# Performance work log

Hardware: AMD Instinct MI355X
Metric: run time of the kernel (lower is better)

## Reference

```python
import jax, jax.numpy as jnp
import numpy as np

H = W = 56
WS = 7            # window size
SHIFT = 3
HEADS = 6
DIM = 192
N = WS * WS       # tokens per window (49)
NW = (H // WS) * (W // WS)  # windows per image (64)
EPS = 1e-5


def _rel_pos_index():
    coords = np.stack(np.meshgrid(np.arange(WS), np.arange(WS), indexing='ij'))
    cf = coords.reshape(2, -1)
    rel = (cf[:, :, None] - cf[:, None, :]).transpose(1, 2, 0)
    rel[:, :, 0] += WS - 1
    rel[:, :, 1] += WS - 1
    rel[:, :, 0] *= 2 * WS - 1
    return rel.sum(-1).astype(np.int32)  # [N, N]


def _attn_mask():
    img = np.zeros([1, H, W, 1], dtype=np.float32)
    slices = (slice(0, -WS), slice(-WS, -SHIFT), slice(-SHIFT, None))
    cnt = 0
    for hs in slices:
        for ws_ in slices:
            img[:, hs, ws_, :] = cnt
            cnt += 1
    m = img.reshape(1, H // WS, WS, W // WS, WS, 1).transpose(0, 1, 3, 2, 4, 5)
    m = m.reshape(-1, N)                      # [nW, N]
    diff = m[:, None, :] - m[:, :, None]
    return np.where(diff != 0, -100.0, 0.0).astype(np.float32)  # [nW, N, N]

_RPI = _rel_pos_index()
_MASK = _attn_mask()


def _ln(x, g, b):
    mu = jnp.mean(x, axis=-1, keepdims=True)
    var = jnp.mean(jnp.square(x - mu), axis=-1, keepdims=True)
    return (x - mu) * jax.lax.rsqrt(var + EPS) * g + b


def setup_inputs() -> dict:
    key = jax.random.key(0)
    ks = jax.random.split(key, 12)
    C, Hd = DIM, DIM * 4
    s = lambda n: 1.0 / np.sqrt(n)
    return {
        'x': jax.random.normal(ks[0], (32, H * W, C), jnp.float32),
        'norm1_g': jnp.ones((C,), jnp.float32),
        'norm1_b': jnp.zeros((C,), jnp.float32),
        'qkv_w': jax.random.normal(ks[1], (C, 3 * C), jnp.float32) * s(C),
        'qkv_b': jnp.zeros((3 * C,), jnp.float32),
        'bias_table': jax.random.normal(ks[2], ((2 * WS - 1) ** 2, HEADS), jnp.float32) * 0.02,
        'proj_w': jax.random.normal(ks[3], (C, C), jnp.float32) * s(C),
        'proj_b': jnp.zeros((C,), jnp.float32),
        'norm2_g': jnp.ones((C,), jnp.float32),
        'norm2_b': jnp.zeros((C,), jnp.float32),
        'fc1_w': jax.random.normal(ks[4], (C, Hd), jnp.float32) * s(C),
        'fc1_b': jnp.zeros((Hd,), jnp.float32),
        'fc2_w': jax.random.normal(ks[5], (Hd, C), jnp.float32) * s(Hd),
        'fc2_b': jnp.zeros((C,), jnp.float32),
    }


def reference(x, norm1_g, norm1_b, qkv_w, qkv_b, bias_table, proj_w, proj_b,
              norm2_g, norm2_b, fc1_w, fc1_b, fc2_w, fc2_b):
    B, L, C = x.shape
    hd = C // HEADS
    scale = hd ** -0.5

    shortcut = x
    h = _ln(x, norm1_g, norm1_b).reshape(B, H, W, C)
    h = jnp.roll(h, (-SHIFT, -SHIFT), axis=(1, 2))

    # window partition -> [B*nW, N, C]
    h = h.reshape(B, H // WS, WS, W // WS, WS, C).transpose(0, 1, 3, 2, 4, 5)
    xw = h.reshape(B * NW, N, C)

    qkv = (xw @ qkv_w + qkv_b).reshape(B * NW, N, 3, HEADS, hd)
    q, k, v = jnp.moveaxis(qkv, 2, 0)                 # each [B*nW, N, H, d]
    q = jnp.swapaxes(q, 1, 2) * scale                 # [B*nW, H, N, d]
    k = jnp.swapaxes(k, 1, 2)
    v = jnp.swapaxes(v, 1, 2)

    attn = jnp.einsum('whnd,whmd->whnm', q, k)        # [B*nW, H, N, N]
    bias = bias_table[jnp.asarray(_RPI).reshape(-1)].reshape(N, N, HEADS)
    attn = attn + jnp.transpose(bias, (2, 0, 1))[None]
    mask = jnp.asarray(_MASK)                         # [nW, N, N]
    attn = attn.reshape(B, NW, HEADS, N, N) + mask[None, :, None]
    attn = jax.nn.softmax(attn.reshape(B * NW, HEADS, N, N), axis=-1)

    out = jnp.einsum('whnm,whmd->whnd', attn, v)      # [B*nW, H, N, d]
    out = jnp.swapaxes(out, 1, 2).reshape(B * NW, N, C)
    out = out @ proj_w + proj_b

    # window reverse -> [B, H, W, C]
    out = out.reshape(B, H // WS, W // WS, WS, WS, C).transpose(0, 1, 3, 2, 4, 5)
    out = out.reshape(B, H, W, C)
    out = jnp.roll(out, (SHIFT, SHIFT), axis=(1, 2)).reshape(B, L, C)

    x = shortcut + out
    hmlp = _ln(x, norm2_g, norm2_b)
    hmlp = jax.nn.gelu(hmlp @ fc1_w + fc1_b, approximate=False) @ fc2_w + fc2_b
    return x + hmlp
```

## Files before the change

kernel.cpp:

```cpp
#include <hip/hip_runtime.h>
#include <hip/hip_bf16.h>
#include <math.h>

static constexpr int CB     = 32;
static constexpr int CH     = 56;
static constexpr int CW     = 56;
static constexpr int CC     = 192;
static constexpr int CSHIFT = 3;
static constexpr int CN     = 49;
static constexpr int CNW    = 64;
static constexpr int CL     = CH * CW;
static constexpr int CM     = CB * CNW * CN;
static constexpr int CHID   = 768;

typedef __attribute__((ext_vector_type(8))) __bf16 bf16x8;
typedef __attribute__((ext_vector_type(4))) float  f32x4;

__device__ __forceinline__ float bfu2f(unsigned short u) {
  union { unsigned i; float f; } c; c.i = (unsigned)u << 16; return c.f;
}
__device__ __forceinline__ unsigned short f2bu(float f) {
  __hip_bfloat16 b = __float2bfloat16(f);
  return *(unsigned short*)&b;
}
__device__ __forceinline__ float gelu_fast(float v) {
  float s  = v * v;
  float u2 = v * fmaf(s, 0.0713548163f, 1.5957691216f);
  float e  = __expf(u2);
  float t  = 1.0f - __fdividef(2.0f, e + 1.0f);
  float h  = 0.5f * v;
  return fmaf(h, t, h);
}

#define GLOAD16(g, l) __builtin_amdgcn_global_load_lds( \
    (__attribute__((address_space(1))) void*)(g),       \
    (__attribute__((address_space(3))) void*)(l), 16, 0, 0)

__global__ __launch_bounds__(256)
void prep_kernel(const float* __restrict__ qkv_w, const float* __restrict__ proj_w,
                 const float* __restrict__ fc1_w, const float* __restrict__ fc2_w,
                 const float* __restrict__ btab,
                 __hip_bfloat16* __restrict__ wq, __hip_bfloat16* __restrict__ wp,
                 __hip_bfloat16* __restrict__ w1, __hip_bfloat16* __restrict__ w2,
                 float* __restrict__ bias2)
{
  int idx = blockIdx.x * 256 + threadIdx.x;
  if (idx < 110592) {
    int k = idx / 576, n = idx - k * 576;
    wq[n * 192 + k] = __float2bfloat16(qkv_w[idx]);
    return;
  }
  idx -= 110592;
  if (idx < 36864) {
    int k = idx / 192, n = idx - k * 192;
    wp[n * 192 + k] = __float2bfloat16(proj_w[idx]);
    return;
  }
  idx -= 36864;
  if (idx < 147456) {
    int k = idx / 768, n = idx - k * 768;
    w1[n * 192 + k] = __float2bfloat16(fc1_w[idx]);
    return;
  }
  idx -= 147456;
  if (idx < 147456) {
    int k = idx / 192, n = idx - k * 192;
    w2[n * 768 + k] = __float2bfloat16(fc2_w[idx]);
    return;
  }
  idx -= 147456;
  if (idx < 98304) {
    int j = idx & 63, i = (idx >> 6) & 63;
    int rest = idx >> 12;
    int h = rest % 6, wt = rest / 6;
    float val;
    if (i >= 49 || j >= 49) {
      val = -INFINITY;
    } else {
      int ti = i / 7, ci = i - ti * 7;
      int tj = j / 7, cj = j - tj * 7;
      val = btab[((ti - tj + 6) * 13 + (ci - cj + 6)) * 6 + h];
      int hri = (wt & 2) ? ((ti < 4) ? 1 : 2) : 0;
      int hci = (wt & 1) ? ((ci < 4) ? 1 : 2) : 0;
      int hrj = (wt & 2) ? ((tj < 4) ? 1 : 2) : 0;
      int hcj = (wt & 1) ? ((cj < 4) ? 1 : 2) : 0;
      if (hri * 3 + hci != hrj * 3 + hcj) val -= 100.0f;
    }
    bias2[idx] = val;
  }
}

template<bool ROLL>
__global__ __launch_bounds__(256)
void ln_kernel(const float* __restrict__ xin, const float* __restrict__ gamma,
               const float* __restrict__ beta, __hip_bfloat16* __restrict__ out)
{
  const int wid = threadIdx.x >> 6, lane = threadIdx.x & 63;
  const int m = blockIdx.x * 4 + wid;
  size_t src;
  if (ROLL) {
    int b   = m / (CNW * CN);
    int rem = m - b * (CNW * CN);
    int nw  = rem / CN, t = rem - nw * CN;
    int wr = nw >> 3, wc = nw & 7;
    int ti = t / 7, tj = t - ti * 7;
    int sr = wr * 7 + ti + CSHIFT; if (sr >= CH) sr -= CH;
    int sc = wc * 7 + tj + CSHIFT; if (sc >= CW) sc -= CW;
    src = ((size_t)b * CL + (size_t)sr * CW + sc) * CC;
  } else {
    src = (size_t)m * CC;
  }
  float v0 = xin[src + lane], v1 = xin[src + lane + 64], v2 = xin[src + lane + 128];
  float s  = v0 + v1 + v2;
  float sq = v0 * v0 + v1 * v1 + v2 * v2;
  #pragma unroll
  for (int off = 32; off; off >>= 1) { s += __shfl_xor(s, off); sq += __shfl_xor(sq, off); }
  const float mu  = s * (1.0f / CC);
  const float inv = rsqrtf(sq * (1.0f / CC) - mu * mu + 1e-5f);
  const size_t dst = (size_t)m * CC;
  out[dst + lane      ] = __float2bfloat16((v0 - mu) * inv * gamma[lane      ] + beta[lane      ]);
  out[dst + lane + 64 ] = __float2bfloat16((v1 - mu) * inv * gamma[lane + 64 ] + beta[lane + 64 ]);
  out[dst + lane + 128] = __float2bfloat16((v2 - mu) * inv * gamma[lane + 128] + beta[lane + 128]);
}

template<int MODE>
__global__ __launch_bounds__(256)
void gemm_mfma(const __hip_bfloat16* __restrict__ Ain, const __hip_bfloat16* __restrict__ Wt,
               const float* __restrict__ bias, void* __restrict__ Outv,
               const float* __restrict__ resid, int K, int Ncols)
{
  __shared__ short As[256 * 64];
  __shared__ short Bs[64 * 64];

  const int tid  = threadIdx.x;
  const int lane = tid & 63, wid = tid >> 6;

  const int nbx = gridDim.x;
  const int nwg = nbx * gridDim.y;
  const int wg  = blockIdx.y * nbx + blockIdx.x;
  const int swz = (wg & 7) * (nwg >> 3) + (wg >> 3);
  const int row0 = (swz / nbx) * 256, col0 = (swz % nbx) * 64;

  const int lr = lane & 15, lg = lane >> 4;

  const short* A  = (const short*)Ain;
  const short* W  = (const short*)Wt;

  f32x4 acc[4][4] = {};

  for (int kk = 0; kk < K; kk += 64) {
    #pragma unroll
    for (int it = 0; it < 8; ++it) {
      int c = it * 256 + tid;
      int row = c >> 3, slot = c & 7;
      int kg = (slot ^ (row & 7)) * 8;
      GLOAD16(A + (size_t)(row0 + row) * K + kk + kg, As + c * 8);
    }
    #pragma unroll
    for (int it = 0; it < 2; ++it) {
      int c = it * 256 + tid;
      int row = c >> 3, slot = c & 7;
      int kg = (slot ^ (row & 7)) * 8;
      GLOAD16(W + (size_t)(col0 + row) * K + kk + kg, Bs + c * 8);
    }
    __syncthreads();

    #pragma unroll
    for (int kh = 0; kh < 2; ++kh) {
      const int sb = kh * 4 + lg;
      bf16x8 bfr[4];
      #pragma unroll
      for (int nt = 0; nt < 4; ++nt) {
        int br = nt * 16 + lr;
        bfr[nt] = *(const bf16x8*)(Bs + br * 64 + (sb ^ (br & 7)) * 8);
      }
      #pragma unroll
      for (int m = 0; m < 4; ++m) {
        int ar = wid * 64 + m * 16 + lr;
        bf16x8 afr = *(const bf16x8*)(As + ar * 64 + (sb ^ (ar & 7)) * 8);
        #pragma unroll
        for (int nt = 0; nt < 4; ++nt)
          acc[m][nt] = __builtin_amdgcn_mfma_f32_16x16x32_bf16(afr, bfr[nt], acc[m][nt], 0, 0, 0);
      }
    }
    __syncthreads();
  }

  float bv[4];
  #pragma unroll
  for (int nt = 0; nt < 4; ++nt) bv[nt] = bias[col0 + nt * 16 + lr];

  #pragma unroll
  for (int m = 0; m < 4; ++m) {
    #pragma unroll
    for (int r = 0; r < 4; ++r) {
      const int mrow = row0 + wid * 64 + m * 16 + lg * 4 + r;
      if (MODE == 0) {
        __hip_bfloat16* O = (__hip_bfloat16*)Outv;
        const size_t rr = (size_t)mrow * Ncols + col0 + lr;
        #pragma unroll
        for (int nt = 0; nt < 4; ++nt)
          O[rr + nt * 16] = __float2bfloat16(acc[m][nt][r] + bv[nt]);
      } else if (MODE == 1) {
        int b = mrow / (CNW * CN);
        int rem = mrow - b * (CNW * CN);
        int nw = rem / CN, t = rem - nw * CN;
        int wr = nw >> 3, wc = nw & 7;
        int ti = t / 7, tj = t - ti * 7;
        int dr = wr * 7 + ti + CSHIFT; if (dr >= CH) dr -= CH;
        int dc = wc * 7 + tj + CSHIFT; if (dc >= CW) dc -= CW;
        const size_t dst = ((size_t)b * CL + (size_t)dr * CW + dc) * CC + col0 + lr;
        float* O = (float*)Outv;
        #pragma unroll
        for (int nt = 0; nt < 4; ++nt)
          O[dst + nt * 16] = resid[dst + nt * 16] + acc[m][nt][r] + bv[nt];
      } else if (MODE == 2) {
        __hip_bfloat16* O = (__hip_bfloat16*)Outv;
        const size_t rr = (size_t)mrow * Ncols + col0 + lr;
        #pragma unroll
        for (int nt = 0; nt < 4; ++nt)
          O[rr + nt * 16] = __float2bfloat16(gelu_fast(acc[m][nt][r] + bv[nt]));
      } else {
        float* O = (float*)Outv;
        const size_t rr = (size_t)mrow * Ncols + col0 + lr;
        #pragma unroll
        for (int nt = 0; nt < 4; ++nt)
          O[rr + nt * 16] = resid[rr + nt * 16] + acc[m][nt][r] + bv[nt];
      }
    }
  }
}

__global__ __launch_bounds__(64)
void attn_mfma_kernel(const __hip_bfloat16* __restrict__ qkv,
                      const float* __restrict__ bias2,
                      __hip_bfloat16* __restrict__ attnout)
{
  __shared__ unsigned short VT[32 * 72];
  __shared__ unsigned short Pl[64 * 72];

  const int bid = blockIdx.x;
  const int w = bid / 6, h = bid - (bid / 6) * 6;
  const int lane = threadIdx.x;
  const int lr = lane & 15, lg = lane >> 4;
  const int nw = w & 63;
  const int wt = (((nw >> 3) == 7) ? 2 : 0) + (((nw & 7) == 7) ? 1 : 0);
  const unsigned short* Q = (const unsigned short*)qkv;
  const size_t rowbase = (size_t)w * 49 * 576;
  const float scale = 0.17677669529663687f;

  for (int e = lane; e < 196; e += 64) {
    int t = e % 49, c = e / 49;
    uint4 v = *(const uint4*)(Q + rowbase + (size_t)t * 576 + 384 + h * 32 + c * 8);
    unsigned va[4] = {v.x, v.y, v.z, v.w};
    #pragma unroll
    for (int q = 0; q < 4; ++q) {
      VT[(c * 8 + q * 2    ) * 72 + t] = (unsigned short)(va[q] & 0xffff);
      VT[(c * 8 + q * 2 + 1) * 72 + t] = (unsigned short)(va[q] >> 16);
    }
  }
  for (int e = lane; e < 32 * 15; e += 64) {
    int d = e / 15, t = 49 + e - (e / 15) * 15;
    VT[d * 72 + t] = 0;
  }

  bf16x8 qf[4], kf[4];
  #pragma unroll
  for (int it = 0; it < 4; ++it) {
    int tok = it * 16 + lr; if (tok > 48) tok = 48;
    qf[it] = *(const bf16x8*)(Q + rowbase + (size_t)tok * 576 + h * 32 + lg * 8);
  }
  #pragma unroll
  for (int jt = 0; jt < 4; ++jt) {
    int tok = jt * 16 + lr; if (tok > 48) tok = 48;
    kf[jt] = *(const bf16x8*)(Q + rowbase + (size_t)tok * 576 + 192 + h * 32 + lg * 8);
  }

  f32x4 acc[4][4] = {};
  #pragma unroll
  for (int jt = 0; jt < 4; ++jt)
    #pragma unroll
    for (int it = 0; it < 4; ++it)
      acc[jt][it] = __builtin_amdgcn_mfma_f32_16x16x32_bf16(kf[jt], qf[it], acc[jt][it], 0, 0, 0);

  __syncthreads();

  const float* brow = bias2 + ((size_t)(wt * 6 + h) * 64) * 64;
  #pragma unroll
  for (int it = 0; it < 4; ++it) {
    const int i = it * 16 + lr;
    float s[4][4];
    #pragma unroll
    for (int jt = 0; jt < 4; ++jt) {
      float4 bv = *(const float4*)(brow + (size_t)i * 64 + jt * 16 + lg * 4);
      s[jt][0] = fmaf(acc[jt][it][0], scale, bv.x);
      s[jt][1] = fmaf(acc[jt][it][1], scale, bv.y);
      s[jt][2] = fmaf(acc[jt][it][2], scale, bv.z);
      s[jt][3] = fmaf(acc[jt][it][3], scale, bv.w);
    }
    float mx = s[0][0];
    #pragma unroll
    for (int jt = 0; jt < 4; ++jt)
      #pragma unroll
      for (int r = 0; r < 4; ++r) mx = fmaxf(mx, s[jt][r]);
    mx = fmaxf(mx, __shfl_xor(mx, 16));
    mx = fmaxf(mx, __shfl_xor(mx, 32));
    float sum = 0.0f;
    #pragma unroll
    for (int jt = 0; jt < 4; ++jt)
      #pragma unroll
      for (int r = 0; r < 4; ++r) { s[jt][r] = __expf(s[jt][r] - mx); sum += s[jt][r]; }
    sum += __shfl_xor(sum, 16);
    sum += __shfl_xor(sum, 32);
    const float inv = 1.0f / sum;
    #pragma unroll
    for (int jt = 0; jt < 4; ++jt) {
      unsigned lo = (unsigned)f2bu(s[jt][0] * inv) | ((unsigned)f2bu(s[jt][1] * inv) << 16);
      unsigned hi = (unsigned)f2bu(s[jt][2] * inv) | ((unsigned)f2bu(s[jt][3] * inv) << 16);
      uint2 val; val.x = lo; val.y = hi;
      *(uint2*)&Pl[i * 72 + jt * 16 + lg * 4] = val;
    }
  }

  __syncthreads();

  f32x4 o[4][2] = {};
  #pragma unroll
  for (int ks = 0; ks < 2; ++ks) {
    bf16x8 pa[4], vb[2];
    #pragma unroll
    for (int it = 0; it < 4; ++it)
      pa[it] = *(const bf16x8*)&Pl[(it * 16 + lr) * 72 + ks * 32 + lg * 8];
    #pragma unroll
    for (int nt = 0; nt < 2; ++nt)
      vb[nt] = *(const bf16x8*)&VT[(nt * 16 + lr) * 72 + ks * 32 + lg * 8];
    #pragma unroll
    for (int it = 0; it < 4; ++it) {
      o[it][0] = __builtin_amdgcn_mfma_f32_16x16x32_bf16(pa[it], vb[0], o[it][0], 0, 0, 0);
      o[it][1] = __builtin_amdgcn_mfma_f32_16x16x32_bf16(pa[it], vb[1], o[it][1], 0, 0, 0);
    }
  }

  #pragma unroll
  for (int it = 0; it < 4; ++it) {
    #pragma unroll
    for (int r = 0; r < 4; ++r) {
      int i = it * 16 + lg * 4 + r;
      if (i < 49) {
        size_t dst = ((size_t)w * 49 + i) * 192 + h * 32;
        attnout[dst + lr]      = __float2bfloat16(o[it][0][r]);
        attnout[dst + 16 + lr] = __float2bfloat16(o[it][1][r]);
      }
    }
  }
}

extern "C" void kernel_launch(void* const* d_in, const int* in_sizes, int n_in,
                              void* d_out, int out_size, void* d_ws, size_t ws_size,
                              hipStream_t stream)
{
  const float* x        = (const float*)d_in[0];
  const float* n1g      = (const float*)d_in[1];
  const float* n1b      = (const float*)d_in[2];
  const float* qkv_w    = (const float*)d_in[3];
  const float* qkv_b    = (const float*)d_in[4];
  const float* btab     = (const float*)d_in[5];
  const float* proj_w   = (const float*)d_in[6];
  const float* proj_b   = (const float*)d_in[7];
  const float* n2g      = (const float*)d_in[8];
  const float* n2b      = (const float*)d_in[9];
  const float* fc1_w    = (const float*)d_in[10];
  const float* fc1_b    = (const float*)d_in[11];
  const float* fc2_w    = (const float*)d_in[12];
  const float* fc2_b    = (const float*)d_in[13];
  float* out = (float*)d_out;

  char* ws = (char*)d_ws;
  const size_t szA = (size_t)CM * CC * 2;
  const size_t szB = (size_t)CM * CHID * 2;
  __hip_bfloat16* bufA = (__hip_bfloat16*)ws;
  __hip_bfloat16* bufB = (__hip_bfloat16*)(ws + szA);
  __hip_bfloat16* wq   = (__hip_bfloat16*)(ws + szA + szB);
  __hip_bfloat16* wp   = wq + 576 * 192;
  __hip_bfloat16* w1   = wp + 192 * 192;
  __hip_bfloat16* w2   = w1 + 768 * 192;
  float* bias2         = (float*)(w2 + 192 * 768);

  prep_kernel<<<(110592 + 36864 + 147456 + 147456 + 98304 + 255) / 256, 256, 0, stream>>>(
      qkv_w, proj_w, fc1_w, fc2_w, btab, wq, wp, w1, w2, bias2);

  ln_kernel<true><<<CM / 4, 256, 0, stream>>>(x, n1g, n1b, bufA);
  gemm_mfma<0><<<dim3(576 / 64, CM / 256), 256, 0, stream>>>(bufA, wq, qkv_b, bufB, nullptr, CC, 576);
  attn_mfma_kernel<<<2048 * 6, 64, 0, stream>>>(bufB, bias2, bufA);
  gemm_mfma<1><<<dim3(192 / 64, CM / 256), 256, 0, stream>>>(bufA, wp, proj_b, out, x, CC, 192);
  ln_kernel<false><<<CM / 4, 256, 0, stream>>>(out, n2g, n2b, bufA);
  gemm_mfma<2><<<dim3(CHID / 64, CM / 256), 256, 0, stream>>>(bufA, w1, fc1_b, bufB, nullptr, CC, CHID);
  gemm_mfma<3><<<dim3(192 / 64, CM / 256), 256, 0, stream>>>(bufB, w2, fc2_b, out, out, CHID, 192);
}
```

Baseline: 369.3 us.

## Replace LDS-staged GEMM with register-direct per-wave 64x64 tiles

The shared-memory tiled GEMM, which used async global-to-LDS loads and block barriers, is replaced by a kernel where each wave independently computes a 64x64 output tile. A and B fragments are loaded straight from global memory into registers with double buffering, and K is now a template parameter so the k-loop fully unrolls. This removes LDS traffic and __syncthreads, but waves no longer share A rows across a block, so global and L2 traffic rises and loads are strided per lane.

New measurement: 511.0 us. +38.4%, slower.

```diff
diff --git a/kernel.cpp b/kernel.cpp
--- a/kernel.cpp
+++ b/kernel.cpp
@@ -31,10 +31,6 @@
   float h  = 0.5f * v;
   return fmaf(h, t, h);
 }
-
-#define GLOAD16(g, l) __builtin_amdgcn_global_load_lds( \
-    (__attribute__((address_space(1))) void*)(g),       \
-    (__attribute__((address_space(3))) void*)(l), 16, 0, 0)
 
 __global__ __launch_bounds__(256)
 void prep_kernel(const float* __restrict__ qkv_w, const float* __restrict__ proj_w,
@@ -123,67 +119,52 @@
   out[dst + lane + 128] = __float2bfloat16((v2 - mu) * inv * gamma[lane + 128] + beta[lane + 128]);
 }
 
-template<int MODE>
+template<int K, int MODE>
 __global__ __launch_bounds__(256)
-void gemm_mfma(const __hip_bfloat16* __restrict__ Ain, const __hip_bfloat16* __restrict__ Wt,
-               const float* __restrict__ bias, void* __restrict__ Outv,
-               const float* __restrict__ resid, int K, int Ncols)
-{
-  __shared__ short As[256 * 64];
-  __shared__ short Bs[64 * 64];
-
-  const int tid  = threadIdx.x;
-  const int lane = tid & 63, wid = tid >> 6;
-
-  const int nbx = gridDim.x;
-  const int nwg = nbx * gridDim.y;
-  const int wg  = blockIdx.y * nbx + blockIdx.x;
-  const int swz = (wg & 7) * (nwg >> 3) + (wg >> 3);
-  const int row0 = (swz / nbx) * 256, col0 = (swz % nbx) * 64;
-
+void gemm_reg(const __hip_bfloat16* __restrict__ Ain, const __hip_bfloat16* __restrict__ Wt,
+              const float* __restrict__ bias, void* __restrict__ Outv,
+              const float* __restrict__ resid, int Ncols)
+{
+  const int tid = threadIdx.x, lane = tid & 63, wid = tid >> 6;
   const int lr = lane & 15, lg = lane >> 4;
 
-  const short* A  = (const short*)Ain;
-  const short* W  = (const short*)Wt;
-
+  const int nb   = gridDim.x;
+  const int sbid = (blockIdx.x & 7) * (nb >> 3) + (blockIdx.x >> 3);
+  const int nbx  = Ncols >> 6;
+  const int t    = sbid * 4 + wid;
+  const int trow = t / nbx;
+  const int row0 = trow * 64, col0 = (t - trow * nbx) * 64;
+
+  const short* A = (const short*)Ain;
+  const short* W = (const short*)Wt;
+  const short* ap = A + (size_t)(row0 + lr) * K + lg * 8;
+  const short* bp = W + (size_t)(col0 + lr) * K + lg * 8;
+
+  constexpr int NK = K / 32;
   f32x4 acc[4][4] = {};
-
-  for (int kk = 0; kk < K; kk += 64) {
-    #pragma unroll
-    for (int it = 0; it < 8; ++it) {
-      int c = it * 256 + tid;
-      int row = c >> 3, slot = c & 7;
-      int kg = (slot ^ (row & 7)) * 8;
-      GLOAD16(A + (size_t)(row0 + row) * K + kk + kg, As + c * 8);
-    }
-    #pragma unroll
-    for (int it = 0; it < 2; ++it) {
-      int c = it * 256 + tid;
-      int row = c >> 3, slot = c & 7;
-      int kg = (slot ^ (row & 7)) * 8;
-      GLOAD16(W + (size_t)(col0 + row) * K + kk + kg, Bs + c * 8);
-    }
-    __syncthreads();
-
-    #pragma unroll
-    for (int kh = 0; kh < 2; ++kh) {
-      const int sb = kh * 4 + lg;
-      bf16x8 bfr[4];
-      #pragma unroll
-      for (int nt = 0; nt < 4; ++nt) {
-        int br = nt * 16 + lr;
-        bfr[nt] = *(const bf16x8*)(Bs + br * 64 + (sb ^ (br & 7)) * 8);
-      }
-      #pragma unroll
-      for (int m = 0; m < 4; ++m) {
-        int ar = wid * 64 + m * 16 + lr;
-        bf16x8 afr = *(const bf16x8*)(As + ar * 64 + (sb ^ (ar & 7)) * 8);
-        #pragma unroll
-        for (int nt = 0; nt < 4; ++nt)
-          acc[m][nt] = __builtin_amdgcn_mfma_f32_16x16x32_bf16(afr, bfr[nt], acc[m][nt], 0, 0, 0);
-      }
-    }
-    __syncthreads();
+  bf16x8 af[2][4], bf[2][4];
+
+  #pragma unroll
+  for (int m = 0; m < 4; ++m) af[0][m] = *(const bf16x8*)(ap + (size_t)m * 16 * K);
+  #pragma unroll
+  for (int n = 0; n < 4; ++n) bf[0][n] = *(const bf16x8*)(bp + (size_t)n * 16 * K);
+
+  #pragma unroll
+  for (int ks = 0; ks < NK; ++ks) {
+    const int cur = ks & 1, nxt = cur ^ 1;
+    if (ks + 1 < NK) {
+      #pragma unroll
+      for (int m = 0; m < 4; ++m)
+        af[nxt][m] = *(const bf16x8*)(ap + (size_t)m * 16 * K + (ks + 1) * 32);
+      #pragma unroll
+      for (int n = 0; n < 4; ++n)
+        bf[nxt][n] = *(const bf16x8*)(bp + (size_t)n * 16 * K + (ks + 1) * 32);
+    }
+    #pragma unroll
+    for (int m = 0; m < 4; ++m)
+      #pragma unroll
+      for (int n = 0; n < 4; ++n)
+        acc[m][n] = __builtin_amdgcn_mfma_f32_16x16x32_bf16(af[cur][m], bf[cur][n], acc[m][n], 0, 0, 0);
   }
 
   float bv[4];
@@ -194,7 +175,7 @@
   for (int m = 0; m < 4; ++m) {
     #pragma unroll
     for (int r = 0; r < 4; ++r) {
-      const int mrow = row0 + wid * 64 + m * 16 + lg * 4 + r;
+      const int mrow = row0 + m * 16 + lg * 4 + r;
       if (MODE == 0) {
         __hip_bfloat16* O = (__hip_bfloat16*)Outv;
         const size_t rr = (size_t)mrow * Ncols + col0 + lr;
@@ -204,9 +185,9 @@
       } else if (MODE == 1) {
         int b = mrow / (CNW * CN);
         int rem = mrow - b * (CNW * CN);
-        int nw = rem / CN, t = rem - nw * CN;
+        int nw = rem / CN, tt = rem - nw * CN;
         int wr = nw >> 3, wc = nw & 7;
-        int ti = t / 7, tj = t - ti * 7;
+        int ti = tt / 7, tj = tt - ti * 7;
         int dr = wr * 7 + ti + CSHIFT; if (dr >= CH) dr -= CH;
         int dc = wc * 7 + tj + CSHIFT; if (dc >= CW) dc -= CW;
         const size_t dst = ((size_t)b * CL + (size_t)dr * CW + dc) * CC + col0 + lr;
@@ -390,10 +371,10 @@
       qkv_w, proj_w, fc1_w, fc2_w, btab, wq, wp, w1, w2, bias2);
 
   ln_kernel<true><<<CM / 4, 256, 0, stream>>>(x, n1g, n1b, bufA);
-  gemm_mfma<0><<<dim3(576 / 64, CM / 256), 256, 0, stream>>>(bufA, wq, qkv_b, bufB, nullptr, CC, 576);
+  gemm_reg<192, 0><<<(CM / 64) * (576 / 64) / 4, 256, 0, stream>>>(bufA, wq, qkv_b, bufB, nullptr, 576);
   attn_mfma_kernel<<<2048 * 6, 64, 0, stream>>>(bufB, bias2, bufA);
-  gemm_mfma<1><<<dim3(192 / 64, CM / 256), 256, 0, stream>>>(bufA, wp, proj_b, out, x, CC, 192);
+  gemm_reg<192, 1><<<(CM / 64) * (192 / 64) / 4, 256, 0, stream>>>(bufA, wp, proj_b, out, x, 192);
   ln_kernel<false><<<CM / 4, 256, 0, stream>>>(out, n2g, n2b, bufA);
-  gemm_mfma<2><<<dim3(CHID / 64, CM / 256), 256, 0, stream>>>(bufA, w1, fc1_b, bufB, nullptr, CC, CHID);
-  gemm_mfma<3><<<dim3(192 / 64, CM / 256), 256, 0, stream>>>(bufB, w2, fc2_b, out, out, CHID, 192);
-}
+  gemm_reg<192, 2><<<(CM / 64) * (CHID / 64) / 4, 256, 0, stream>>>(bufA, w1, fc1_b, bufB, nullptr, CHID);
+  gemm_reg<768, 3><<<(CM / 64) * (192 / 64) / 4, 256, 0, stream>>>(bufB, w2, fc2_b, out, out, 192);
+}
```

## Retile GEMMs to 128-row blocks with 2x2 warp layout and compile-time shapes

Applied to the files above, without the earlier changes.

The GEMM kernel moves from 256x64 tiles, where each warp owns 64 rows by 64 columns, to 128xBN tiles (BN of 128 or 64) with a 2x2 warp grid. K and N become template parameters so the K loop can be fully unrolled. The QKV output is padded from 576 to 640 columns, with zeroed weights and bias, so its N divides by 128, and the attention kernel's row stride is changed to match. This aims to raise the number of workgroups and improve occupancy, at the cost of the extra padded QKV columns and a larger QKV buffer.

Result: faster. 349.3 us (-5.4%).

```diff
diff --git a/kernel.cpp b/kernel.cpp
--- a/kernel.cpp
+++ b/kernel.cpp
@@ -12,6 +12,7 @@
 static constexpr int CL     = CH * CW;
 static constexpr int CM     = CB * CNW * CN;
 static constexpr int CHID   = 768;
+static constexpr int QST    = 640;
 
 typedef __attribute__((ext_vector_type(8))) __bf16 bf16x8;
 typedef __attribute__((ext_vector_type(4))) float  f32x4;
@@ -39,18 +40,18 @@
 __global__ __launch_bounds__(256)
 void prep_kernel(const float* __restrict__ qkv_w, const float* __restrict__ proj_w,
                  const float* __restrict__ fc1_w, const float* __restrict__ fc2_w,
-                 const float* __restrict__ btab,
+                 const float* __restrict__ btab, const float* __restrict__ qkv_b,
                  __hip_bfloat16* __restrict__ wq, __hip_bfloat16* __restrict__ wp,
                  __hip_bfloat16* __restrict__ w1, __hip_bfloat16* __restrict__ w2,
-                 float* __restrict__ bias2)
+                 float* __restrict__ bias2, float* __restrict__ qkv_bp)
 {
   int idx = blockIdx.x * 256 + threadIdx.x;
-  if (idx < 110592) {
-    int k = idx / 576, n = idx - k * 576;
-    wq[n * 192 + k] = __float2bfloat16(qkv_w[idx]);
+  if (idx < QST * 192) {
+    int n = idx / 192, k = idx - n * 192;
+    wq[idx] = (n < 576) ? __float2bfloat16(qkv_w[k * 576 + n]) : __float2bfloat16(0.0f);
     return;
   }
-  idx -= 110592;
+  idx -= QST * 192;
   if (idx < 36864) {
     int k = idx / 192, n = idx - k * 192;
     wp[n * 192 + k] = __float2bfloat16(proj_w[idx]);
@@ -87,6 +88,11 @@
       if (hri * 3 + hci != hrj * 3 + hcj) val -= 100.0f;
     }
     bias2[idx] = val;
+    return;
+  }
+  idx -= 98304;
+  if (idx < QST) {
+    qkv_bp[idx] = (idx < 576) ? qkv_b[idx] : 0.0f;
   }
 }
 
@@ -123,41 +129,44 @@
   out[dst + lane + 128] = __float2bfloat16((v2 - mu) * inv * gamma[lane + 128] + beta[lane + 128]);
 }
 
-template<int MODE>
+template<int K, int N, int BN, int MODE>
 __global__ __launch_bounds__(256)
 void gemm_mfma(const __hip_bfloat16* __restrict__ Ain, const __hip_bfloat16* __restrict__ Wt,
                const float* __restrict__ bias, void* __restrict__ Outv,
-               const float* __restrict__ resid, int K, int Ncols)
+               const float* __restrict__ resid)
 {
-  __shared__ short As[256 * 64];
-  __shared__ short Bs[64 * 64];
+  constexpr int NT = BN / 32;
+  __shared__ short As[128 * 64];
+  __shared__ short Bs[BN * 64];
 
   const int tid  = threadIdx.x;
   const int lane = tid & 63, wid = tid >> 6;
 
-  const int nbx = gridDim.x;
+  const int nbx = N / BN;
   const int nwg = nbx * gridDim.y;
   const int wg  = blockIdx.y * nbx + blockIdx.x;
   const int swz = (wg & 7) * (nwg >> 3) + (wg >> 3);
-  const int row0 = (swz / nbx) * 256, col0 = (swz % nbx) * 64;
-
+  const int row0 = (swz / nbx) * 128, col0 = (swz % nbx) * BN;
+
+  const int wm = wid >> 1, wn = wid & 1;
   const int lr = lane & 15, lg = lane >> 4;
 
   const short* A  = (const short*)Ain;
   const short* W  = (const short*)Wt;
 
-  f32x4 acc[4][4] = {};
-
+  f32x4 acc[4][NT] = {};
+
+  #pragma unroll
   for (int kk = 0; kk < K; kk += 64) {
     #pragma unroll
-    for (int it = 0; it < 8; ++it) {
+    for (int it = 0; it < 4; ++it) {
       int c = it * 256 + tid;
       int row = c >> 3, slot = c & 7;
       int kg = (slot ^ (row & 7)) * 8;
       GLOAD16(A + (size_t)(row0 + row) * K + kk + kg, As + c * 8);
     }
     #pragma unroll
-    for (int it = 0; it < 2; ++it) {
+    for (int it = 0; it < BN / 32; ++it) {
       int c = it * 256 + tid;
       int row = c >> 3, slot = c & 7;
       int kg = (slot ^ (row & 7)) * 8;
@@ -168,38 +177,39 @@
     #pragma unroll
     for (int kh = 0; kh < 2; ++kh) {
       const int sb = kh * 4 + lg;
-      bf16x8 bfr[4];
+      bf16x8 bfr[NT];
       #pragma unroll
-      for (int nt = 0; nt < 4; ++nt) {
-        int br = nt * 16 + lr;
+      for (int nt = 0; nt < NT; ++nt) {
+        int br = wn * (BN / 2) + nt * 16 + lr;
         bfr[nt] = *(const bf16x8*)(Bs + br * 64 + (sb ^ (br & 7)) * 8);
       }
       #pragma unroll
       for (int m = 0; m < 4; ++m) {
-        int ar = wid * 64 + m * 16 + lr;
+        int ar = wm * 64 + m * 16 + lr;
         bf16x8 afr = *(const bf16x8*)(As + ar * 64 + (sb ^ (ar & 7)) * 8);
         #pragma unroll
-        for (int nt = 0; nt < 4; ++nt)
+        for (int nt = 0; nt < NT; ++nt)
           acc[m][nt] = __builtin_amdgcn_mfma_f32_16x16x32_bf16(afr, bfr[nt], acc[m][nt], 0, 0, 0);
       }
     }
     __syncthreads();
   }
 
-  float bv[4];
-  #pragma unroll
-  for (int nt = 0; nt < 4; ++nt) bv[nt] = bias[col0 + nt * 16 + lr];
+  const int colA = col0 + wn * (BN / 2) + lr;
+  float bv[NT];
+  #pragma unroll
+  for (int nt = 0; nt < NT; ++nt) bv[nt] = bias[colA + nt * 16];
 
   #pragma unroll
   for (int m = 0; m < 4; ++m) {
     #pragma unroll
     for (int r = 0; r < 4; ++r) {
-      const int mrow = row0 + wid * 64 + m * 16 + lg * 4 + r;
+      const int mrow = row0 + wm * 64 + m * 16 + lg * 4 + r;
       if (MODE == 0) {
         __hip_bfloat16* O = (__hip_bfloat16*)Outv;
-        const size_t rr = (size_t)mrow * Ncols + col0 + lr;
+        const size_t rr = (size_t)mrow * N + colA;
         #pragma unroll
-        for (int nt = 0; nt < 4; ++nt)
+        for (int nt = 0; nt < NT; ++nt)
           O[rr + nt * 16] = __float2bfloat16(acc[m][nt][r] + bv[nt]);
       } else if (MODE == 1) {
         int b = mrow / (CNW * CN);
@@ -209,22 +219,22 @@
         int ti = t / 7, tj = t - ti * 7;
         int dr = wr * 7 + ti + CSHIFT; if (dr >= CH) dr -= CH;
         int dc = wc * 7 + tj + CSHIFT; if (dc >= CW) dc -= CW;
-        const size_t dst = ((size_t)b * CL + (size_t)dr * CW + dc) * CC + col0 + lr;
+        const size_t dst = ((size_t)b * CL + (size_t)dr * CW + dc) * CC + colA;
         float* O = (float*)Outv;
         #pragma unroll
-        for (int nt = 0; nt < 4; ++nt)
+        for (int nt = 0; nt < NT; ++nt)
           O[dst + nt * 16] = resid[dst + nt * 16] + acc[m][nt][r] + bv[nt];
       } else if (MODE == 2) {
         __hip_bfloat16* O = (__hip_bfloat16*)Outv;
-        const size_t rr = (size_t)mrow * Ncols + col0 + lr;
+        const size_t rr = (size_t)mrow * N + colA;
         #pragma unroll
-        for (int nt = 0; nt < 4; ++nt)
+        for (int nt = 0; nt < NT; ++nt)
           O[rr + nt * 16] = __float2bfloat16(gelu_fast(acc[m][nt][r] + bv[nt]));
       } else {
         float* O = (float*)Outv;
-        const size_t rr = (size_t)mrow * Ncols + col0 + lr;
+        const size_t rr = (size_t)mrow * N + colA;
         #pragma unroll
-        for (int nt = 0; nt < 4; ++nt)
+        for (int nt = 0; nt < NT; ++nt)
           O[rr + nt * 16] = resid[rr + nt * 16] + acc[m][nt][r] + bv[nt];
       }
     }
@@ -246,12 +256,12 @@
   const int nw = w & 63;
   const int wt = (((nw >> 3) == 7) ? 2 : 0) + (((nw & 7) == 7) ? 1 : 0);
   const unsigned short* Q = (const unsigned short*)qkv;
-  const size_t rowbase = (size_t)w * 49 * 576;
+  const size_t rowbase = (size_t)w * 49 * QST;
   const float scale = 0.17677669529663687f;
 
   for (int e = lane; e < 196; e += 64) {
     int t = e % 49, c = e / 49;
-    uint4 v = *(const uint4*)(Q + rowbase + (size_t)t * 576 + 384 + h * 32 + c * 8);
+    uint4 v = *(const uint4*)(Q + rowbase + (size_t)t * QST + 384 + h * 32 + c * 8);
     unsigned va[4] = {v.x, v.y, v.z, v.w};
     #pragma unroll
     for (int q = 0; q < 4; ++q) {
@@ -268,12 +278,12 @@
   #pragma unroll
   for (int it = 0; it < 4; ++it) {
     int tok = it * 16 + lr; if (tok > 48) tok = 48;
-    qf[it] = *(const bf16x8*)(Q + rowbase + (size_t)tok * 576 + h * 32 + lg * 8);
+    qf[it] = *(const bf16x8*)(Q + rowbase + (size_t)tok * QST + h * 32 + lg * 8);
   }
   #pragma unroll
   for (int jt = 0; jt < 4; ++jt) {
     int tok = jt * 16 + lr; if (tok > 48) tok = 48;
-    kf[jt] = *(const bf16x8*)(Q + rowbase + (size_t)tok * 576 + 192 + h * 32 + lg * 8);
+    kf[jt] = *(const bf16x8*)(Q + rowbase + (size_t)tok * QST + 192 + h * 32 + lg * 8);
   }
 
   f32x4 acc[4][4] = {};
@@ -381,19 +391,21 @@
   __hip_bfloat16* bufA = (__hip_bfloat16*)ws;
   __hip_bfloat16* bufB = (__hip_bfloat16*)(ws + szA);
   __hip_bfloat16* wq   = (__hip_bfloat16*)(ws + szA + szB);
-  __hip_bfloat16* wp   = wq + 576 * 192;
+  __hip_bfloat16* wp   = wq + QST * 192;
   __hip_bfloat16* w1   = wp + 192 * 192;
   __hip_bfloat16* w2   = w1 + 768 * 192;
   float* bias2         = (float*)(w2 + 192 * 768);
-
-  prep_kernel<<<(110592 + 36864 + 147456 + 147456 + 98304 + 255) / 256, 256, 0, stream>>>(
-      qkv_w, proj_w, fc1_w, fc2_w, btab, wq, wp, w1, w2, bias2);
+  float* qkv_bp        = bias2 + 98304;
+
+  const int prep_total = QST * 192 + 36864 + 147456 + 147456 + 98304 + QST;
+  prep_kernel<<<(prep_total + 255) / 256, 256, 0, stream>>>(
+      qkv_w, proj_w, fc1_w, fc2_w, btab, qkv_b, wq, wp, w1, w2, bias2, qkv_bp);
 
   ln_kernel<true><<<CM / 4, 256, 0, stream>>>(x, n1g, n1b, bufA);
-  gemm_mfma<0><<<dim3(576 / 64, CM / 256), 256, 0, stream>>>(bufA, wq, qkv_b, bufB, nullptr, CC, 576);
+  gemm_mfma<192, QST, 128, 0><<<dim3(QST / 128, CM / 128), 256, 0, stream>>>(bufA, wq, qkv_bp, bufB, nullptr);
   attn_mfma_kernel<<<2048 * 6, 64, 0, stream>>>(bufB, bias2, bufA);
-  gemm_mfma<1><<<dim3(192 / 64, CM / 256), 256, 0, stream>>>(bufA, wp, proj_b, out, x, CC, 192);
+  gemm_mfma<192, 192, 64, 1><<<dim3(192 / 64, CM / 128), 256, 0, stream>>>(bufA, wp, proj_b, out, x);
   ln_kernel<false><<<CM / 4, 256, 0, stream>>>(out, n2g, n2b, bufA);
-  gemm_mfma<2><<<dim3(CHID / 64, CM / 256), 256, 0, stream>>>(bufA, w1, fc1_b, bufB, nullptr, CC, CHID);
-  gemm_mfma<3><<<dim3(192 / 64, CM / 256), 256, 0, stream>>>(bufB, w2, fc2_b, out, out, CHID, 192);
-}
+  gemm_mfma<192, CHID, 128, 2><<<dim3(CHID / 128, CM / 128), 256, 0, stream>>>(bufA, w1, fc1_b, bufB, nullptr);
+  gemm_mfma<CHID, 192, 64, 3><<<dim3(192 / 64, CM / 128), 256, 0, stream>>>(bufB, w2, fc2_b, out, out);
+}
```
